# Kernel tuning notes

Measured on AMD Instinct MI355X. Metric: run time of the kernel, lower is better.

Reference implementation:

```python
import jax, jax.numpy as jnp
import numpy as np

B, C, T = 128, 9, 2048
R = T // 4            # reduced_timesteps after two MaxPool1d(2)
N = B * R             # total graph nodes
E_SINGLE = 8192       # edges per sample graph (avg degree 16 over R nodes)
HID = 128
OUT = 12


def setup_inputs():
    key = jax.random.key(0)
    ks = jax.random.split(key, 14)
    x = jax.random.normal(ks[0], (B, C, T), jnp.float32)
    # per-sample graph, replicated with offset i*R per batch element (as in forward)
    single = jax.random.randint(ks[1], (2, E_SINGLE), 0, R)
    offsets = (jnp.arange(B) * R)[None, :, None]
    edge_index = (single[:, None, :] + offsets).reshape(2, -1)  # [2, B*E_SINGLE]

    def lin(k, fan_in, shape):
        return jax.random.normal(k, shape, jnp.float32) / np.sqrt(fan_in)

    return {
        "x": x,
        "edge_index": edge_index,
        "conv1_w": lin(ks[2], C * 5, (16, C, 5)),
        "conv1_b": jnp.zeros((16,), jnp.float32),
        "conv2_w": lin(ks[3], 16 * 5, (32, 16, 5)),
        "conv2_b": jnp.zeros((32,), jnp.float32),
        "gcn1_w": lin(ks[4], 32, (32, HID)),
        "gcn1_b": jnp.zeros((HID,), jnp.float32),
        "gcn2_w": lin(ks[5], HID, (HID, HID)),
        "gcn2_b": jnp.zeros((HID,), jnp.float32),
        "fc_w": lin(ks[6], HID, (HID, OUT)),
        "fc_b": jnp.zeros((OUT,), jnp.float32),
    }


def _gcn_conv(h, edge_index, w, b, n):
    # PyG GCNConv: linear -> add self-loops -> sym-normalized sum aggregation -> + bias
    h = h @ w
    loops = jnp.arange(n)
    row = jnp.concatenate([edge_index[0], loops])  # source
    col = jnp.concatenate([edge_index[1], loops])  # target (aggregation)
    deg = jax.ops.segment_sum(jnp.ones(col.shape, h.dtype), col, num_segments=n)
    dis = jnp.where(deg > 0, jax.lax.rsqrt(jnp.maximum(deg, 1e-12)), 0.0)
    norm = dis[row] * dis[col]                      # [E+N]
    out = jax.ops.segment_sum(norm[:, None] * h[row], col, num_segments=n)
    return out + b


def _temporal_conv(x, w1, b1, w2, b2):
    dn = ("NCH", "OIH", "NCH")
    h = jax.lax.conv_general_dilated(x, w1, (1,), [(2, 2)], dimension_numbers=dn)
    h = jax.nn.relu(h + b1[None, :, None])
    h = jax.lax.reduce_window(h, -jnp.inf, jax.lax.max, (1, 1, 2), (1, 1, 2), "VALID")
    h = jax.lax.conv_general_dilated(h, w2, (1,), [(2, 2)], dimension_numbers=dn)
    h = jax.nn.relu(h + b2[None, :, None])
    h = jax.lax.reduce_window(h, -jnp.inf, jax.lax.max, (1, 1, 2), (1, 1, 2), "VALID")
    return h  # [B, 32, R]


def reference(x, edge_index, conv1_w, conv1_b, conv2_w, conv2_b,
              gcn1_w, gcn1_b, gcn2_w, gcn2_b, fc_w, fc_b):
    h = _temporal_conv(x, conv1_w, conv1_b, conv2_w, conv2_b)   # [B, 32, R]
    nodes = h.transpose(0, 2, 1).reshape(B * R, 32)             # [N, 32]
    g = jax.nn.relu(_gcn_conv(nodes, edge_index, gcn1_w, gcn1_b, N))
    g = jax.nn.relu(_gcn_conv(g, edge_index, gcn2_w, gcn2_b, N))
    g = g.reshape(B, R, HID).mean(axis=1)                       # [B, HID]
    return g @ fc_w + fc_b                                      # [B, OUT]
```

## Files before the change

### kernel.cpp

```cpp
#include <hip/hip_runtime.h>
#include <hip/hip_bf16.h>

#define BB   128
#define CIN  9
#define TT   2048
#define RR   512
#define NN   (BB*RR)
#define HID  128
#define NOUT 12

typedef __attribute__((ext_vector_type(8))) short short8;
typedef __attribute__((ext_vector_type(4))) float f32x4;

static __device__ inline unsigned short f2bf(float f) {
    unsigned int u = __float_as_uint(f);
    unsigned int r = (u + 0x7fffu + ((u >> 16) & 1u)) >> 16;
    return (unsigned short)r;
}
static __device__ inline float bf2f(unsigned short u) {
    return __uint_as_float(((unsigned int)u) << 16);
}

__global__ __launch_bounds__(512) void k_convs(const float* __restrict__ x,
        const float* __restrict__ w1, const float* __restrict__ b1,
        const float* __restrict__ w2, const float* __restrict__ b2,
        unsigned short* __restrict__ nodesT,
        const int* __restrict__ ei, int E, int es,
        unsigned short* __restrict__ Ab16,
        const float* __restrict__ g2w, unsigned short* __restrict__ w2t,
        float* __restrict__ meanbuf, int* __restrict__ done) {
    __shared__ __align__(16) union {
        struct { float sx[CIN][268]; float s1[16][132]; } c;
        struct { int cnt[512]; float arow[8][512]; } a;
    } u;
    int tid = threadIdx.x;
    int bid = blockIdx.x;

    if (bid == 0) {
        float4 z = make_float4(0.f, 0.f, 0.f, 0.f);
        for (int i = tid; i < 128 * 128 / 4; i += 512) ((float4*)meanbuf)[i] = z;
        if (tid < 128) done[tid] = 0;
        for (int idx = tid; idx < 128 * 128; idx += 512) {
            int c2 = idx >> 7, f = idx & 127;
            w2t[f * 128 + c2] = f2bf(g2w[idx]);
        }
        return;
    }

    if (bid <= 64) {
        int base = (bid - 1) * 8;
        u.a.cnt[tid] = 0;
        float4 z = make_float4(0.f, 0.f, 0.f, 0.f);
        float4* az = (float4*)u.a.arow;
        az[tid] = z; az[tid + 512] = z;
        __syncthreads();
        for (int i = tid; i < es; i += 512) atomicAdd(&u.a.cnt[ei[E + i]], 1);
        __syncthreads();
        for (int i = tid; i < es; i += 512) {
            int c = ei[E + i];
            if (c >= base && c < base + 8) {
                int r = ei[i];
                float nd = rsqrtf((float)u.a.cnt[r] + 1.0f);
                float dn = rsqrtf((float)u.a.cnt[c] + 1.0f);
                atomicAdd(&u.a.arow[c - base][r], nd * dn);
            }
        }
        if (tid < 8) {
            int r = base + tid;
            float d = rsqrtf((float)u.a.cnt[r] + 1.0f);
            atomicAdd(&u.a.arow[tid][r], d * d);
        }
        __syncthreads();
        {
            int row = tid >> 6, c0 = (tid & 63) * 8;
            const float* p = &u.a.arow[row][c0];
            ushort4 o0, o1;
            o0.x = f2bf(p[0]); o0.y = f2bf(p[1]); o0.z = f2bf(p[2]); o0.w = f2bf(p[3]);
            o1.x = f2bf(p[4]); o1.y = f2bf(p[5]); o1.z = f2bf(p[6]); o1.w = f2bf(p[7]);
            *(ushort4*)&Ab16[(size_t)(base + row) * 512 + c0]     = o0;
            *(ushort4*)&Ab16[(size_t)(base + row) * 512 + c0 + 4] = o1;
        }
        return;
    }

    int cb = bid - 65;
    int b  = cb >> 3;
    int r0 = (cb & 7) * 64;
    int wv   = __builtin_amdgcn_readfirstlane(tid >> 6);
    int lane = tid & 63;

    for (int idx = tid; idx < CIN * 268; idx += 512) {
        int c = idx / 268, j = idx - c * 268;
        int g = 4 * r0 - 6 + j;
        float v = 0.f;
        if (g >= 0 && g < TT) v = x[(b * CIN + c) * TT + g];
        u.c.sx[c][j] = v;
    }
    __syncthreads();

    {
        int c1a = wv * 2, c1b = wv * 2 + 1;
        float biasA = b1[c1a], biasB = b1[c1b];
        for (int pp = lane; pp < 132; pp += 64) {
            int p = 2 * r0 - 2 + pp;
            float valA = 0.f, valB = 0.f;
            if (p >= 0 && p < 1024) {
                float a0A = biasA, a1A = biasA, a0B = biasB, a1B = biasB;
#pragma unroll
                for (int c = 0; c < CIN; ++c) {
                    const float2* px = (const float2*)&u.c.sx[c][2 * pp];
                    float2 q0 = px[0], q1 = px[1], q2 = px[2];
                    {
                        const float* wp = &w1[(c1a * CIN + c) * 5];
                        float k0 = wp[0], k1 = wp[1], k2 = wp[2], k3 = wp[3], k4 = wp[4];
                        a0A += q0.x*k0 + q0.y*k1 + q1.x*k2 + q1.y*k3 + q2.x*k4;
                        a1A += q0.y*k0 + q1.x*k1 + q1.y*k2 + q2.x*k3 + q2.y*k4;
                    }
                    {
                        const float* wp = &w1[(c1b * CIN + c) * 5];
                        float k0 = wp[0], k1 = wp[1], k2 = wp[2], k3 = wp[3], k4 = wp[4];
                        a0B += q0.x*k0 + q0.y*k1 + q1.x*k2 + q1.y*k3 + q2.x*k4;
                        a1B += q0.y*k0 + q1.x*k1 + q1.y*k2 + q2.x*k3 + q2.y*k4;
                    }
                }
                valA = fmaxf(fmaxf(a0A, a1A), 0.f);
                valB = fmaxf(fmaxf(a0B, a1B), 0.f);
            }
            u.c.s1[c1a][pp] = valA;
            u.c.s1[c1b][pp] = valB;
        }
    }
    __syncthreads();

    int rl = lane;
    float acc0[4], acc1[4];
#pragma unroll
    for (int o = 0; o < 4; ++o) {
        float bv = b2[wv * 4 + o];
        acc0[o] = bv; acc1[o] = bv;
    }
#pragma unroll
    for (int c = 0; c < 16; ++c) {
        const float2* ps = (const float2*)&u.c.s1[c][2 * rl];
        float2 q0 = ps[0], q1 = ps[1], q2 = ps[2];
#pragma unroll
        for (int o = 0; o < 4; ++o) {
            const float* wp = &w2[((wv * 4 + o) * 16 + c) * 5];
            float k0 = wp[0], k1 = wp[1], k2 = wp[2], k3 = wp[3], k4 = wp[4];
            acc0[o] += q0.x*k0 + q0.y*k1 + q1.x*k2 + q1.y*k3 + q2.x*k4;
            acc1[o] += q0.y*k0 + q1.x*k1 + q1.y*k2 + q2.x*k3 + q2.y*k4;
        }
    }
    int n = r0 + rl;
    unsigned short* np = nodesT + ((size_t)b * 32 + wv * 4) * 512 + n;
    np[0]    = f2bf(fmaxf(fmaxf(acc0[0], acc1[0]), 0.f));
    np[512]  = f2bf(fmaxf(fmaxf(acc0[1], acc1[1]), 0.f));
    np[1024] = f2bf(fmaxf(fmaxf(acc0[2], acc1[2]), 0.f));
    np[1536] = f2bf(fmaxf(fmaxf(acc0[3], acc1[3]), 0.f));
}

__global__ __launch_bounds__(256) void k_agg1(const unsigned short* __restrict__ Ab,
        const unsigned short* __restrict__ nT, const float* __restrict__ w1,
        const float* __restrict__ b1, unsigned short* __restrict__ h16) {
    __shared__ unsigned short sA[128][72];
    __shared__ unsigned short sN[32][72];
    __shared__ float sAgg[128][33];
    __shared__ float sw1[32 * 128];
    int tid = threadIdx.x;
    int b  = blockIdx.x >> 2;
    int rb = blockIdx.x & 3;
    int r0 = rb * 128;
    const unsigned short* nb = nT + (size_t)b * 32 * 512;

    {
        const float4* src = (const float4*)w1;
        float4* dst = (float4*)sw1;
#pragma unroll
        for (int i = 0; i < 4; ++i) dst[tid + i * 256] = src[tid + i * 256];
    }

    int wv = tid >> 6, lane = tid & 63;
    int l15 = lane & 15, quad = lane >> 4;
    int mB = wv * 32;
    f32x4 acc[2][2];
#pragma unroll
    for (int i = 0; i < 2; ++i)
#pragma unroll
        for (int j = 0; j < 2; ++j) acc[i][j] = (f32x4){0.f, 0.f, 0.f, 0.f};

    for (int kt = 0; kt < 8; ++kt) {
        int k0 = kt * 64;
        __syncthreads();
#pragma unroll
        for (int i = 0; i < 8; ++i) {
            int idx = tid + i * 256;
            int row = idx >> 4, c4 = (idx & 15) * 4;
            *(ushort4*)&sA[row][c4] = *(const ushort4*)&Ab[(size_t)(r0 + row) * 512 + k0 + c4];
        }
#pragma unroll
        for (int i = 0; i < 2; ++i) {
            int idx = tid + i * 256;
            int f = idx >> 4, c4 = (idx & 15) * 4;
            *(ushort4*)&sN[f][c4] = *(const ushort4*)&nb[(size_t)f * 512 + k0 + c4];
        }
        __syncthreads();
#pragma unroll
        for (int ks = 0; ks < 2; ++ks) {
            int kk = ks * 32 + quad * 8;
            short8 av0 = *(const short8*)&sA[mB + l15][kk];
            short8 av1 = *(const short8*)&sA[mB + 16 + l15][kk];
            short8 bv0 = *(const short8*)&sN[l15][kk];
            short8 bv1 = *(const short8*)&sN[16 + l15][kk];
            acc[0][0] = __builtin_amdgcn_mfma_f32_16x16x32_bf16(av0, bv0, acc[0][0], 0, 0, 0);
            acc[0][1] = __builtin_amdgcn_mfma_f32_16x16x32_bf16(av0, bv1, acc[0][1], 0, 0, 0);
            acc[1][0] = __builtin_amdgcn_mfma_f32_16x16x32_bf16(av1, bv0, acc[1][0], 0, 0, 0);
            acc[1][1] = __builtin_amdgcn_mfma_f32_16x16x32_bf16(av1, bv1, acc[1][1], 0, 0, 0);
        }
    }
    __syncthreads();
#pragma unroll
    for (int mi = 0; mi < 2; ++mi)
#pragma unroll
        for (int ni = 0; ni < 2; ++ni)
#pragma unroll
            for (int r = 0; r < 4; ++r)
                sAgg[mB + mi * 16 + quad * 4 + r][ni * 16 + l15] = acc[mi][ni][r];
    __syncthreads();

    int fq = tid & 31;
    int ng = tid >> 5;
    float4 bv = *(const float4*)&b1[fq * 4];
    for (int ch = 0; ch < 4; ++ch) {
        float a[4][4];
#pragma unroll
        for (int j = 0; j < 4; ++j)
#pragma unroll
            for (int q = 0; q < 4; ++q) a[j][q] = 0.f;
#pragma unroll
        for (int c = 0; c < 32; ++c) {
            float4 wvv = *(const float4*)&sw1[c * 128 + fq * 4];
#pragma unroll
            for (int j = 0; j < 4; ++j) {
                float xc = sAgg[ch * 32 + ng * 4 + j][c];
                a[j][0] += xc * wvv.x; a[j][1] += xc * wvv.y;
                a[j][2] += xc * wvv.z; a[j][3] += xc * wvv.w;
            }
        }
#pragma unroll
        for (int j = 0; j < 4; ++j) {
            ushort4 o;
            o.x = f2bf(fmaxf(a[j][0] + bv.x, 0.f));
            o.y = f2bf(fmaxf(a[j][1] + bv.y, 0.f));
            o.z = f2bf(fmaxf(a[j][2] + bv.z, 0.f));
            o.w = f2bf(fmaxf(a[j][3] + bv.w, 0.f));
            *(ushort4*)&h16[(size_t)(b * 512 + r0 + ch * 32 + ng * 4 + j) * 128 + fq * 4] = o;
        }
    }
}

__global__ __launch_bounds__(256) void k_lin2(const unsigned short* __restrict__ g16,
        const unsigned short* __restrict__ w2t, unsigned short* __restrict__ tT) {
    __shared__ __align__(16) unsigned short smem2[64 * 136 + 128 * 136];
    unsigned short (*srow)[136] = (unsigned short (*)[136])smem2;
    unsigned short (*swT)[136]  = (unsigned short (*)[136])&smem2[64 * 136];
    unsigned short (*sOut)[72]  = (unsigned short (*)[72])smem2;
    int tid = threadIdx.x;
    int nbase = blockIdx.x * 64;

    {
        const ushort4* src = (const ushort4*)(g16 + (size_t)nbase * 128);
#pragma unroll
        for (int i = 0; i < 8; ++i) {
            int idx = tid + i * 256;
            int row = idx >> 5, col4 = idx & 31;
            ushort4 v = src[idx];
            *(ushort4*)&srow[row][col4 * 4] = v;
        }
    }
    {
        const ushort4* src = (const ushort4*)w2t;
#pragma unroll
        for (int i = 0; i < 16; ++i) {
            int idx = tid + i * 256;
            int f = idx >> 5, c4 = idx & 31;
            ushort4 v = src[idx];
            *(ushort4*)&swT[f][c4 * 4] = v;
        }
    }
    __syncthreads();

    int wv  = tid >> 6;
    int lane = tid & 63;
    int m0 = wv * 16;
    int l15 = lane & 15;
    int quad = lane >> 4;
    f32x4 acc[8];
#pragma unroll
    for (int nt = 0; nt < 8; ++nt) acc[nt] = (f32x4){0.f, 0.f, 0.f, 0.f};
#pragma unroll
    for (int kc = 0; kc < 4; ++kc) {
        int k0 = kc * 32 + quad * 8;
        short8 a = *(const short8*)&srow[m0 + l15][k0];
#pragma unroll
        for (int nt = 0; nt < 8; ++nt) {
            short8 b = *(const short8*)&swT[nt * 16 + l15][k0];
            acc[nt] = __builtin_amdgcn_mfma_f32_16x16x32_bf16(a, b, acc[nt], 0, 0, 0);
        }
    }
    __syncthreads();

#pragma unroll
    for (int nt = 0; nt < 8; ++nt) {
        ushort4 o;
        o.x = f2bf(acc[nt][0]); o.y = f2bf(acc[nt][1]);
        o.z = f2bf(acc[nt][2]); o.w = f2bf(acc[nt][3]);
        *(ushort4*)&sOut[nt * 16 + l15][m0 + quad * 4] = o;
    }
    __syncthreads();

    int b = nbase >> 9;
    int rl0 = nbase & 511;
#pragma unroll
    for (int i = 0; i < 8; ++i) {
        int idx = tid + i * 256;
        int col = idx >> 4, r4 = (idx & 15) * 4;
        ushort4 v = *(ushort4*)&sOut[col][r4];
        *(ushort4*)&tT[((size_t)(b * 128 + col)) * 512 + rl0 + r4] = v;
    }
}

__global__ __launch_bounds__(256) void k_agg2(const unsigned short* __restrict__ Ab,
        const unsigned short* __restrict__ tT, const float* __restrict__ b2,
        float* __restrict__ meanbuf, int* __restrict__ done,
        const float* __restrict__ fw, const float* __restrict__ fb,
        float* __restrict__ out) {
    __shared__ unsigned short sA[2][128][72];
    __shared__ unsigned short sB[2][128][72];
    __shared__ float sred[2][128];
    __shared__ float sm[HID];
    __shared__ int slast;
    int tid = threadIdx.x;
    int b  = blockIdx.x >> 2;
    int rb = blockIdx.x & 3;
    int r0 = rb * 128;
    const unsigned short* tb = tT + (size_t)b * 128 * 512;
    int wv = tid >> 6, lane = tid & 63;
    int l15 = lane & 15, quad = lane >> 4;
    int wr = wv >> 1, wc = wv & 1;
    f32x4 acc[4][4];
#pragma unroll
    for (int i = 0; i < 4; ++i)
#pragma unroll
        for (int j = 0; j < 4; ++j) acc[i][j] = (f32x4){0.f, 0.f, 0.f, 0.f};

    ushort4 stA[8], stB[8];
#pragma unroll
    for (int i = 0; i < 8; ++i) {
        int idx = tid + i * 256;
        int row = idx >> 4, c4 = (idx & 15) * 4;
        stA[i] = *(const ushort4*)&Ab[(size_t)(r0 + row) * 512 + c4];
        stB[i] = *(const ushort4*)&tb[(size_t)row * 512 + c4];
    }

    int cur = 0;
    for (int kt = 0; kt < 8; ++kt) {
#pragma unroll
        for (int i = 0; i < 8; ++i) {
            int idx = tid + i * 256;
            int row = idx >> 4, c4 = (idx & 15) * 4;
            *(ushort4*)&sA[cur][row][c4] = stA[i];
            *(ushort4*)&sB[cur][row][c4] = stB[i];
        }
        __syncthreads();
        if (kt < 7) {
            int k0 = (kt + 1) * 64;
#pragma unroll
            for (int i = 0; i < 8; ++i) {
                int idx = tid + i * 256;
                int row = idx >> 4, c4 = (idx & 15) * 4;
                stA[i] = *(const ushort4*)&Ab[(size_t)(r0 + row) * 512 + k0 + c4];
                stB[i] = *(const ushort4*)&tb[(size_t)row * 512 + k0 + c4];
            }
        }
#pragma unroll
        for (int ks = 0; ks < 2; ++ks) {
            int kk = ks * 32 + quad * 8;
            short8 av[4], bfr[4];
#pragma unroll
            for (int mi = 0; mi < 4; ++mi)
                av[mi] = *(const short8*)&sA[cur][wr * 64 + mi * 16 + l15][kk];
#pragma unroll
            for (int ni = 0; ni < 4; ++ni)
                bfr[ni] = *(const short8*)&sB[cur][wc * 64 + ni * 16 + l15][kk];
#pragma unroll
            for (int mi = 0; mi < 4; ++mi)
#pragma unroll
                for (int ni = 0; ni < 4; ++ni)
                    acc[mi][ni] = __builtin_amdgcn_mfma_f32_16x16x32_bf16(av[mi], bfr[ni], acc[mi][ni], 0, 0, 0);
        }
        cur ^= 1;
    }

#pragma unroll
    for (int ni = 0; ni < 4; ++ni) {
        int col = wc * 64 + ni * 16 + l15;
        float bc = b2[col];
        float s = 0.f;
#pragma unroll
        for (int mi = 0; mi < 4; ++mi)
#pragma unroll
            for (int r = 0; r < 4; ++r)
                s += fmaxf(acc[mi][ni][r] + bc, 0.f);
        s += __shfl_xor(s, 16);
        s += __shfl_xor(s, 32);
        if (quad == 0) sred[wr][col] = s;
    }
    __syncthreads();
    if (tid < 128)
        atomicAdd(&meanbuf[b * 128 + tid], (sred[0][tid] + sred[1][tid]) * (1.0f / RR));
    __syncthreads();
    if (tid == 0) {
        __threadfence();
        slast = (atomicAdd(&done[b], 1) == 3) ? 1 : 0;
    }
    __syncthreads();
    if (slast) {
        __threadfence();
        if (tid < HID)
            sm[tid] = __hip_atomic_load(&meanbuf[b * 128 + tid],
                                        __ATOMIC_RELAXED, __HIP_MEMORY_SCOPE_AGENT);
        __syncthreads();
        if (tid < NOUT) {
            float s = fb[tid];
#pragma unroll
            for (int c = 0; c < HID; ++c) s += sm[c] * fw[c * NOUT + tid];
            out[b * NOUT + tid] = s;
        }
    }
}

extern "C" void kernel_launch(void* const* d_in, const int* in_sizes, int n_in,
                              void* d_out, int out_size, void* d_ws, size_t ws_size,
                              hipStream_t stream) {
    const float* x   = (const float*)d_in[0];
    const int*   ei  = (const int*)d_in[1];
    const float* c1w = (const float*)d_in[2];
    const float* c1b = (const float*)d_in[3];
    const float* c2w = (const float*)d_in[4];
    const float* c2b = (const float*)d_in[5];
    const float* g1w = (const float*)d_in[6];
    const float* g1b = (const float*)d_in[7];
    const float* g2w = (const float*)d_in[8];
    const float* g2b = (const float*)d_in[9];
    const float* fw  = (const float*)d_in[10];
    const float* fb  = (const float*)d_in[11];
    float* out = (float*)d_out;
    int E  = in_sizes[1] / 2;
    int es = E / BB;

    char* ws = (char*)d_ws;
    unsigned short* nodesT = (unsigned short*)(ws);
    unsigned short* h1     = (unsigned short*)(ws + (4u << 20));
    unsigned short* tT     = (unsigned short*)(ws + (20u << 20));
    unsigned short* Ab16   = (unsigned short*)(ws + (37u << 20));
    float* meanbuf         = (float*)(ws + (37u << 20) + (512u << 10));
    int*   done            = (int*)  (ws + (37u << 20) + (576u << 10));
    unsigned short* w2t    = (unsigned short*)(ws + (37u << 20) + (772u << 10));

    k_convs<<<1089, 512, 0, stream>>>(x, c1w, c1b, c2w, c2b, nodesT,
                                      ei, E, es, Ab16, g2w, w2t, meanbuf, done);

    k_agg1<<<512, 256, 0, stream>>>(Ab16, nodesT, g1w, g1b, h1);

    k_lin2<<<NN / 64, 256, 0, stream>>>(h1, w2t, tT);
    k_agg2<<<512, 256, 0, stream>>>(Ab16, tT, g2b, meanbuf, done, fw, fb, out);
}
```

Measured before the change: 176.7 us.

## Fuse GCN layer-1 aggregation with layer-2 linear and double-buffer adjacency tiles

Merges the layer-1 aggregation kernel and the layer-2 linear kernel into one, so the layer-1 hidden activations stay in shared memory and the h1 global round trip and one launch go away. It also double-buffers the adjacency and node tiles in LDS and prefetches the next K tile into registers while the current one runs through MFMA. In exchange LDS use rises to about 79KB per block, which may lower occupancy. The w2t fragments are now read straight from global memory instead of being staged in LDS.

```diff
diff --git a/kernel.cpp b/kernel.cpp
--- a/kernel.cpp
+++ b/kernel.cpp
@@ -159,13 +159,18 @@
     np[1536] = f2bf(fmaxf(fmaxf(acc0[3], acc1[3]), 0.f));
 }
 
-__global__ __launch_bounds__(256) void k_agg1(const unsigned short* __restrict__ Ab,
+__global__ __launch_bounds__(256) void k_l1l2(const unsigned short* __restrict__ Ab,
         const unsigned short* __restrict__ nT, const float* __restrict__ w1,
-        const float* __restrict__ b1, unsigned short* __restrict__ h16) {
-    __shared__ unsigned short sA[128][72];
-    __shared__ unsigned short sN[32][72];
-    __shared__ float sAgg[128][33];
-    __shared__ float sw1[32 * 128];
+        const float* __restrict__ b1, const unsigned short* __restrict__ w2t,
+        unsigned short* __restrict__ tT) {
+    __shared__ __align__(16) char smem[79360];
+    unsigned short* sAp  = (unsigned short*)smem;
+    unsigned short* sNp  = (unsigned short*)(smem + 36864);
+    float*          sAgg = (float*)(smem + 46080);
+    float*          sw1  = (float*)(smem + 62976);
+    unsigned short* h1L  = (unsigned short*)smem;
+    unsigned short* sOutH= (unsigned short*)(smem + 36864);
+
     int tid = threadIdx.x;
     int b  = blockIdx.x >> 2;
     int rb = blockIdx.x & 3;
@@ -188,43 +193,70 @@
 #pragma unroll
         for (int j = 0; j < 2; ++j) acc[i][j] = (f32x4){0.f, 0.f, 0.f, 0.f};
 
+    ushort4 stA[8], stB[2];
+#pragma unroll
+    for (int i = 0; i < 8; ++i) {
+        int idx = tid + i * 256;
+        int row = idx >> 4, c4 = (idx & 15) * 4;
+        stA[i] = *(const ushort4*)&Ab[(size_t)(r0 + row) * 512 + c4];
+    }
+#pragma unroll
+    for (int i = 0; i < 2; ++i) {
+        int idx = tid + i * 256;
+        int f = idx >> 4, c4 = (idx & 15) * 4;
+        stB[i] = *(const ushort4*)&nb[(size_t)f * 512 + c4];
+    }
+    int cur = 0;
     for (int kt = 0; kt < 8; ++kt) {
-        int k0 = kt * 64;
-        __syncthreads();
 #pragma unroll
         for (int i = 0; i < 8; ++i) {
             int idx = tid + i * 256;
             int row = idx >> 4, c4 = (idx & 15) * 4;
-            *(ushort4*)&sA[row][c4] = *(const ushort4*)&Ab[(size_t)(r0 + row) * 512 + k0 + c4];
+            *(ushort4*)&sAp[(size_t)cur * 9216 + row * 72 + c4] = stA[i];
         }
 #pragma unroll
         for (int i = 0; i < 2; ++i) {
             int idx = tid + i * 256;
             int f = idx >> 4, c4 = (idx & 15) * 4;
-            *(ushort4*)&sN[f][c4] = *(const ushort4*)&nb[(size_t)f * 512 + k0 + c4];
-        }
-        __syncthreads();
+            *(ushort4*)&sNp[(size_t)cur * 2304 + f * 72 + c4] = stB[i];
+        }
+        __syncthreads();
+        if (kt < 7) {
+            int k0 = (kt + 1) * 64;
+#pragma unroll
+            for (int i = 0; i < 8; ++i) {
+                int idx = tid + i * 256;
+                int row = idx >> 4, c4 = (idx & 15) * 4;
+                stA[i] = *(const ushort4*)&Ab[(size_t)(r0 + row) * 512 + k0 + c4];
+            }
+#pragma unroll
+            for (int i = 0; i < 2; ++i) {
+                int idx = tid + i * 256;
+                int f = idx >> 4, c4 = (idx & 15) * 4;
+                stB[i] = *(const ushort4*)&nb[(size_t)f * 512 + k0 + c4];
+            }
+        }
 #pragma unroll
         for (int ks = 0; ks < 2; ++ks) {
             int kk = ks * 32 + quad * 8;
-            short8 av0 = *(const short8*)&sA[mB + l15][kk];
-            short8 av1 = *(const short8*)&sA[mB + 16 + l15][kk];
-            short8 bv0 = *(const short8*)&sN[l15][kk];
-            short8 bv1 = *(const short8*)&sN[16 + l15][kk];
+            short8 av0 = *(const short8*)&sAp[(size_t)cur * 9216 + (mB + l15) * 72 + kk];
+            short8 av1 = *(const short8*)&sAp[(size_t)cur * 9216 + (mB + 16 + l15) * 72 + kk];
+            short8 bv0 = *(const short8*)&sNp[(size_t)cur * 2304 + l15 * 72 + kk];
+            short8 bv1 = *(const short8*)&sNp[(size_t)cur * 2304 + (16 + l15) * 72 + kk];
             acc[0][0] = __builtin_amdgcn_mfma_f32_16x16x32_bf16(av0, bv0, acc[0][0], 0, 0, 0);
             acc[0][1] = __builtin_amdgcn_mfma_f32_16x16x32_bf16(av0, bv1, acc[0][1], 0, 0, 0);
             acc[1][0] = __builtin_amdgcn_mfma_f32_16x16x32_bf16(av1, bv0, acc[1][0], 0, 0, 0);
             acc[1][1] = __builtin_amdgcn_mfma_f32_16x16x32_bf16(av1, bv1, acc[1][1], 0, 0, 0);
         }
-    }
-    __syncthreads();
+        cur ^= 1;
+    }
 #pragma unroll
     for (int mi = 0; mi < 2; ++mi)
 #pragma unroll
         for (int ni = 0; ni < 2; ++ni)
 #pragma unroll
             for (int r = 0; r < 4; ++r)
-                sAgg[mB + mi * 16 + quad * 4 + r][ni * 16 + l15] = acc[mi][ni][r];
+                sAgg[(mB + mi * 16 + quad * 4 + r) * 33 + ni * 16 + l15] = acc[mi][ni][r];
     __syncthreads();
 
     int fq = tid & 31;
@@ -241,91 +273,56 @@
             float4 wvv = *(const float4*)&sw1[c * 128 + fq * 4];
 #pragma unroll
             for (int j = 0; j < 4; ++j) {
-                float xc = sAgg[ch * 32 + ng * 4 + j][c];
+                float xc = sAgg[(ch * 32 + ng * 4 + j) * 33 + c];
                 a[j][0] += xc * wvv.x; a[j][1] += xc * wvv.y;
                 a[j][2] += xc * wvv.z; a[j][3] += xc * wvv.w;
             }
         }
 #pragma unroll
         for (int j = 0; j < 4; ++j) {
+            int row = ch * 32 + ng * 4 + j;
             ushort4 o;
             o.x = f2bf(fmaxf(a[j][0] + bv.x, 0.f));
             o.y = f2bf(fmaxf(a[j][1] + bv.y, 0.f));
             o.z = f2bf(fmaxf(a[j][2] + bv.z, 0.f));
             o.w = f2bf(fmaxf(a[j][3] + bv.w, 0.f));
-            *(ushort4*)&h16[(size_t)(b * 512 + r0 + ch * 32 + ng * 4 + j) * 128 + fq * 4] = o;
-        }
-    }
-}
-
-__global__ __launch_bounds__(256) void k_lin2(const unsigned short* __restrict__ g16,
-        const unsigned short* __restrict__ w2t, unsigned short* __restrict__ tT) {
-    __shared__ __align__(16) unsigned short smem2[64 * 136 + 128 * 136];
-    unsigned short (*srow)[136] = (unsigned short (*)[136])smem2;
-    unsigned short (*swT)[136]  = (unsigned short (*)[136])&smem2[64 * 136];
-    unsigned short (*sOut)[72]  = (unsigned short (*)[72])smem2;
-    int tid = threadIdx.x;
-    int nbase = blockIdx.x * 64;
-
-    {
-        const ushort4* src = (const ushort4*)(g16 + (size_t)nbase * 128);
+            *(ushort4*)&h1L[row * 136 + fq * 4] = o;
+        }
+    }
+    __syncthreads();
+
+    for (int h = 0; h < 2; ++h) {
+        int m0 = h * 64 + wv * 16;
+        f32x4 acc2[8];
+#pragma unroll
+        for (int nt = 0; nt < 8; ++nt) acc2[nt] = (f32x4){0.f, 0.f, 0.f, 0.f};
+#pragma unroll
+        for (int kc = 0; kc < 4; ++kc) {
+            int k0 = kc * 32 + quad * 8;
+            short8 af = *(const short8*)&h1L[(m0 + l15) * 136 + k0];
+#pragma unroll
+            for (int nt = 0; nt < 8; ++nt) {
+                short8 bfr = *(const short8*)&w2t[(size_t)(nt * 16 + l15) * 128 + k0];
+                acc2[nt] = __builtin_amdgcn_mfma_f32_16x16x32_bf16(af, bfr, acc2[nt], 0, 0, 0);
+            }
+        }
+        __syncthreads();
+#pragma unroll
+        for (int nt = 0; nt < 8; ++nt) {
+            ushort4 o;
+            o.x = f2bf(acc2[nt][0]); o.y = f2bf(acc2[nt][1]);
+            o.z = f2bf(acc2[nt][2]); o.w = f2bf(acc2[nt][3]);
+            *(ushort4*)&sOutH[(nt * 16 + l15) * 72 + wv * 16 + quad * 4] = o;
+        }
+        __syncthreads();
 #pragma unroll
         for (int i = 0; i < 8; ++i) {
             int idx = tid + i * 256;
-            int row = idx >> 5, col4 = idx & 31;
-            ushort4 v = src[idx];
-            *(ushort4*)&srow[row][col4 * 4] = v;
-        }
-    }
-    {
-        const ushort4* src = (const ushort4*)w2t;
-#pragma unroll
-        for (int i = 0; i < 16; ++i) {
-            int idx = tid + i * 256;
-            int f = idx >> 5, c4 = idx & 31;
-            ushort4 v = src[idx];
-            *(ushort4*)&swT[f][c4 * 4] = v;
-        }
-    }
-    __syncthreads();
-
-    int wv  = tid >> 6;
-    int lane = tid & 63;
-    int m0 = wv * 16;
-    int l15 = lane & 15;
-    int quad = lane >> 4;
-    f32x4 acc[8];
-#pragma unroll
-    for (int nt = 0; nt < 8; ++nt) acc[nt] = (f32x4){0.f, 0.f, 0.f, 0.f};
-#pragma unroll
-    for (int kc = 0; kc < 4; ++kc) {
-        int k0 = kc * 32 + quad * 8;
-        short8 a = *(const short8*)&srow[m0 + l15][k0];
-#pragma unroll
-        for (int nt = 0; nt < 8; ++nt) {
-            short8 b = *(const short8*)&swT[nt * 16 + l15][k0];
-            acc[nt] = __builtin_amdgcn_mfma_f32_16x16x32_bf16(a, b, acc[nt], 0, 0, 0);
-        }
-    }
-    __syncthreads();
-
-#pragma unroll
-    for (int nt = 0; nt < 8; ++nt) {
-        ushort4 o;
-        o.x = f2bf(acc[nt][0]); o.y = f2bf(acc[nt][1]);
-        o.z = f2bf(acc[nt][2]); o.w = f2bf(acc[nt][3]);
-        *(ushort4*)&sOut[nt * 16 + l15][m0 + quad * 4] = o;
-    }
-    __syncthreads();
-
-    int b = nbase >> 9;
-    int rl0 = nbase & 511;
-#pragma unroll
-    for (int i = 0; i < 8; ++i) {
-        int idx = tid + i * 256;
-        int col = idx >> 4, r4 = (idx & 15) * 4;
-        ushort4 v = *(ushort4*)&sOut[col][r4];
-        *(ushort4*)&tT[((size_t)(b * 128 + col)) * 512 + rl0 + r4] = v;
+            int f = idx >> 4, n4 = (idx & 15) * 4;
+            ushort4 v = *(ushort4*)&sOutH[f * 72 + n4];
+            *(ushort4*)&tT[((size_t)(b * 128 + f)) * 512 + r0 + h * 64 + n4] = v;
+        }
+        __syncthreads();
     }
 }
 
@@ -460,7 +457,6 @@
 
     char* ws = (char*)d_ws;
     unsigned short* nodesT = (unsigned short*)(ws);
-    unsigned short* h1     = (unsigned short*)(ws + (4u << 20));
     unsigned short* tT     = (unsigned short*)(ws + (20u << 20));
     unsigned short* Ab16   = (unsigned short*)(ws + (37u << 20));
     float* meanbuf         = (float*)(ws + (37u << 20) + (512u << 10));
@@ -470,8 +466,7 @@
     k_convs<<<1089, 512, 0, stream>>>(x, c1w, c1b, c2w, c2b, nodesT,
                                       ei, E, es, Ab16, g2w, w2t, meanbuf, done);
 
-    k_agg1<<<512, 256, 0, stream>>>(Ab16, nodesT, g1w, g1b, h1);
-
-    k_lin2<<<NN / 64, 256, 0, stream>>>(h1, w2t, tT);
+    k_l1l2<<<512, 256, 0, stream>>>(Ab16, nodesT, g1w, g1b, w2t, tT);
+
     k_agg2<<<512, 256, 0, stream>>>(Ab16, tT, g2b, meanbuf, done, fw, fb, out);
 }
```

Result: no change. 175.7 us (-0.6%).
